# Performance work log

Measured on AMD Instinct MI355X. Metric: run time of the kernel, lower is better.

Reference implementation:

```python
import jax, jax.numpy as jnp
import numpy as np
import math

B, T, C = 2, 2048, 1024
H, DK, DV = 16, 64, 64


def setup_inputs() -> dict:
    key = jax.random.key(0)
    ks = jax.random.split(key, 5)
    # randw(*d) = randn(*d) / sqrt(d[-1])
    x = jax.random.normal(ks[0], (B, T, C), dtype=jnp.float32)
    w_q = jax.random.normal(ks[1], (H, DK, C), dtype=jnp.float32) / math.sqrt(C)
    w_k = jax.random.normal(ks[2], (H, DK, C), dtype=jnp.float32) / math.sqrt(C)
    w_v = jax.random.normal(ks[3], (H, DV, C), dtype=jnp.float32) / math.sqrt(C)
    w_o = jax.random.normal(ks[4], (H * DV, C), dtype=jnp.float32) / math.sqrt(C)
    return {"x": x, "w_q": w_q, "w_k": w_k, "w_v": w_v, "w_o": w_o}


def reference(x, w_q, w_k, w_v, w_o):
    # Full prefill: bs_q.first = 0, bs_q.nb = T, causal=True, dropout=0 (eval).
    dk = w_q.shape[1]
    q = jnp.einsum('ntc,hdc->nhtd', x, w_q)  # [B,H,T,DK]
    k = jnp.einsum('ntc,hdc->nhtd', x, w_k)  # [B,H,T,DK]
    v = jnp.einsum('ntc,hdc->nhtd', x, w_v)  # [B,H,T,DV]
    a = jnp.einsum('nhtd,nhsd->nhts', q, k) / jnp.sqrt(jnp.asarray(dk, x.dtype))
    # amm_generator: mask where query_idx < key_idx (strict upper triangle)
    t = a.shape[-1]
    mask = jnp.arange(t)[:, None] < jnp.arange(t)[None, :]  # [T,T] bool
    a = jnp.where(mask[None, None], jnp.asarray(-jnp.inf, a.dtype), a)
    a = jax.nn.softmax(a, axis=-1)
    y = jnp.einsum('nhts,nhsd->nthd', a, v)  # [B,T,H,DV]
    y = y.reshape(y.shape[0], y.shape[1], -1)  # [B,T,H*DV]
    return y @ w_o  # [B,T,C]
```

## Files before the change

kernel.cpp:

```cpp
#include <hip/hip_runtime.h>
#include <hip/hip_bf16.h>

#define B_ 2
#define T_ 2048
#define C_ 1024
#define H_ 16
#define D_ 64

typedef __attribute__((ext_vector_type(8))) short bf16x8;
typedef __attribute__((ext_vector_type(4))) float f32x4;
typedef __attribute__((ext_vector_type(8))) unsigned short u16x8;
typedef __attribute__((ext_vector_type(2))) unsigned int u32x2;
typedef __attribute__((ext_vector_type(4))) unsigned int u32x4;

__device__ __forceinline__ unsigned short bf1(float a) {
    __bf16 x = (__bf16)a;
    return __builtin_bit_cast(unsigned short, x);
}
__device__ __forceinline__ unsigned int pk2(float a, float b) {
    return (unsigned int)bf1(a) | ((unsigned int)bf1(b) << 16);
}
__device__ __forceinline__ float bf2f(unsigned short u) {
    union { unsigned int u; float f; } v; v.u = (unsigned int)u << 16;
    return v.f;
}

__device__ __forceinline__ void gll16(const void* g, void* l) {
    __builtin_amdgcn_global_load_lds(
        (const __attribute__((address_space(1))) unsigned int*)g,
        (__attribute__((address_space(3))) unsigned int*)l, 16, 0, 0);
}

__global__ __launch_bounds__(256) void prep_x(
    const float* __restrict__ x, unsigned short* __restrict__ xb)
{
    const size_t i = ((size_t)blockIdx.x * 256 + threadIdx.x) * 16;
    float4 f0 = *reinterpret_cast<const float4*>(x + i);
    float4 f1 = *reinterpret_cast<const float4*>(x + i + 4);
    float4 f2 = *reinterpret_cast<const float4*>(x + i + 8);
    float4 f3 = *reinterpret_cast<const float4*>(x + i + 12);
    u32x4 a = {pk2(f0.x, f0.y), pk2(f0.z, f0.w), pk2(f1.x, f1.y), pk2(f1.z, f1.w)};
    u32x4 b = {pk2(f2.x, f2.y), pk2(f2.z, f2.w), pk2(f3.x, f3.y), pk2(f3.z, f3.w)};
    *reinterpret_cast<u32x4*>(xb + i) = a;
    *reinterpret_cast<u32x4*>(xb + i + 8) = b;
}

__global__ __launch_bounds__(256) void prep_w(
    const float* __restrict__ wq, const float* __restrict__ wk,
    const float* __restrict__ wv, unsigned short* __restrict__ wb)
{
    const int bid = blockIdx.x, tid = threadIdx.x;
    const int rb = bid * 4;
    const float* src = (rb < 1024) ? wq + (size_t)rb * 1024
                     : (rb < 2048) ? wk + (size_t)(rb - 1024) * 1024
                                   : wv + (size_t)(rb - 2048) * 1024;
    const float sc = (rb < 1024) ? 0.125f * 1.4426950408889634f : 1.0f;
    const float4* s4 = (const float4*)src;
    u32x2* d = (u32x2*)(wb + (size_t)rb * 1024);
#pragma unroll
    for (int k = 0; k < 4; k++) {
        float4 v = s4[k * 256 + tid];
        u32x2 w;
        w[0] = pk2(v.x * sc, v.y * sc);
        w[1] = pk2(v.z * sc, v.w * sc);
        d[k * 256 + tid] = w;
    }
}

__global__ __launch_bounds__(256) void prep_wo(
    const float* __restrict__ wo, unsigned short* __restrict__ wt)
{
    __shared__ unsigned short tile[64][72];
    const int tk = (blockIdx.x & 15) << 6, tn = (blockIdx.x >> 4) << 6;
    const int r = threadIdx.x >> 2, cb = (threadIdx.x & 3) << 4;
#pragma unroll
    for (int j = 0; j < 4; j++) {
        float4 v = *reinterpret_cast<const float4*>(
            wo + (size_t)(tk + r) * 1024 + tn + cb + j * 4);
        u32x2 w;
        w[0] = pk2(v.x, v.y);
        w[1] = pk2(v.z, v.w);
        *reinterpret_cast<u32x2*>(&tile[r][cb + j * 4]) = w;
    }
    __syncthreads();
    unsigned short buf[16];
#pragma unroll
    for (int j = 0; j < 16; j++) buf[j] = tile[cb + j][r];
    unsigned short* dst = wt + (size_t)(tn + r) * 1024 + tk + cb;
    *reinterpret_cast<u16x8*>(dst) = *reinterpret_cast<u16x8*>(buf);
    *reinterpret_cast<u16x8*>(dst + 8) = *reinterpret_cast<u16x8*>(buf + 8);
}

__global__ __launch_bounds__(256) void qkv_gemm(
    const unsigned short* __restrict__ xb, const unsigned short* __restrict__ wb,
    unsigned short* __restrict__ qkv)
{
    __shared__ __align__(16) unsigned short As[2][128 * 64];
    __shared__ __align__(16) unsigned short Bs[2][128 * 64];
    const int tid = threadIdx.x;
    const int lane = tid & 63, wave = tid >> 6;
    const int g = lane >> 4, c16 = lane & 15;
    const int xcd = blockIdx.x & 7, idx = blockIdx.x >> 3;
    const int bm = (xcd << 2) + idx / 24, bn = idx % 24;
    const int jbase = bn << 7;
    const int which = jbase >> 10;

    const int srow = wave * 32 + (lane >> 3);
    const int swc = ((lane & 7) ^ (lane >> 3)) << 3;
    const unsigned short* asrc = xb + ((size_t)(bm << 7) + srow) * C_ + swc;
    const unsigned short* bsrc = wb + ((size_t)(bn << 7) + srow) * C_ + swc;

    f32x4 acc[4][4];
#pragma unroll
    for (int i = 0; i < 4; i++)
#pragma unroll
        for (int j = 0; j < 4; j++) acc[i][j] = (f32x4){0.f, 0.f, 0.f, 0.f};

    const int wm = (wave >> 1) << 6, wn = (wave & 1) << 6;

    auto stage = [&](int buf, int k0) {
#pragma unroll
        for (int i = 0; i < 4; i++) {
            gll16(asrc + k0 + i * 8 * C_, &As[buf][(wave * 32 + i * 8) << 6]);
            gll16(bsrc + k0 + i * 8 * C_, &Bs[buf][(wave * 32 + i * 8) << 6]);
        }
    };

    stage(0, 0);
    int cur = 0;
    for (int t = 0; t < 16; ++t) {
        __syncthreads();
        if (t < 15) stage(cur ^ 1, (t + 1) << 6);
#pragma unroll
        for (int kk = 0; kk < 2; kk++) {
            bf16x8 af[4], bfv[4];
#pragma unroll
            for (int m = 0; m < 4; m++)
                af[m] = *reinterpret_cast<const bf16x8*>(
                    &As[cur][((wm + m * 16 + c16) << 6) + ((((kk << 2) + g) ^ (c16 & 7)) << 3)]);
#pragma unroll
            for (int n = 0; n < 4; n++)
                bfv[n] = *reinterpret_cast<const bf16x8*>(
                    &Bs[cur][((wn + n * 16 + c16) << 6) + ((((kk << 2) + g) ^ (c16 & 7)) << 3)]);
#pragma unroll
            for (int m = 0; m < 4; m++)
#pragma unroll
                for (int n = 0; n < 4; n++)
                    acc[m][n] = __builtin_amdgcn_mfma_f32_16x16x32_bf16(af[m], bfv[n], acc[m][n], 0, 0, 0);
        }
        cur ^= 1;
    }

    if (which < 2) {
#pragma unroll
        for (int m = 0; m < 4; m++) {
            const int grow = (bm << 7) + wm + m * 16 + (g << 2);
#pragma unroll
            for (int n = 0; n < 4; n++) {
                const int jj = (jbase + wn + n * 16 + c16) & 1023;
                const int h = jj >> 6, d = jj & 63;
#pragma unroll
                for (int r = 0; r < 4; r++) {
                    const int row = grow + r;
                    const int b = row >> 11, t = row & 2047;
                    const size_t off = ((size_t)((which * B_ + b) * H_ + h) * T_ + t) * 64 + d;
                    qkv[off] = bf1(acc[m][n][r]);
                }
            }
        }
    } else {
#pragma unroll
        for (int m = 0; m < 4; m++) {
            const int grow = (bm << 7) + wm + m * 16 + (g << 2);
            const int b = grow >> 11, t = grow & 2047;
#pragma unroll
            for (int n = 0; n < 4; n++) {
                const int jj = (jbase + wn + n * 16 + c16) & 1023;
                const int h = jj >> 6, d = jj & 63;
                u32x2 w;
                w[0] = pk2(acc[m][n][0], acc[m][n][1]);
                w[1] = pk2(acc[m][n][2], acc[m][n][3]);
                const size_t off = ((size_t)((2 * B_ + b) * H_ + h) * 64 + d) * T_ + t;
                *reinterpret_cast<u32x2*>(&qkv[off]) = w;
            }
        }
    }
}

__global__ __launch_bounds__(256) void attn(
    const unsigned short* __restrict__ qkv,
    unsigned short* __restrict__ opA, unsigned short* __restrict__ opB,
    float* __restrict__ lbuf)
{
    __shared__ __align__(16) unsigned short Ks[2][64 * 64];
    __shared__ __align__(16) unsigned short Vt[2][64 * 64];
    __shared__ __align__(16) unsigned short Ps[4][16 * 64];
    const int tid = threadIdx.x, lane = tid & 63, wave = tid >> 6;
    const int g = lane >> 4, c16 = lane & 15;
    const int qt = 31 - (blockIdx.x >> 6);
    const int rem = blockIdx.x & 63;
    const int half = rem >> 5, bh = rem & 31;
    const int b = bh >> 4, h = bh & 15;
    const size_t headoff = (size_t)(b * H_ + h) * T_ * 64;
    const size_t QSZ = (size_t)B_ * H_ * T_ * 64;
    const unsigned short* qp = qkv + headoff;
    const unsigned short* kp = qkv + QSZ + headoff;
    const unsigned short* vTp = qkv + 2 * QSZ + headoff;

    const int nt = qt + 1;
    const int h1 = (nt + 1) >> 1;
    const int itlo = half ? h1 : 0, ithi = half ? nt : h1;

    const int qbase = (qt << 6) + wave * 16;
    bf16x8 qf0, qf1;
    {
        const size_t r0 = (size_t)(qbase + c16) * 64;
        qf0 = *reinterpret_cast<const bf16x8*>(qp + r0 + g * 8);
        qf1 = *reinterpret_cast<const bf16x8*>(qp + r0 + 32 + g * 8);
    }

    float l_lane = 0.f;
    f32x4 acc[4];
#pragma unroll
    for (int i = 0; i < 4; i++) acc[i] = (f32x4){0.f, 0.f, 0.f, 0.f};

    const int srow8 = lane >> 3;
    const int swc = ((lane & 7) ^ srow8) << 3;
    const unsigned short* ksrc = kp + (size_t)(wave * 16 + srow8) * 64 + swc;
    const unsigned short* vsrc = vTp + (size_t)(wave * 16 + srow8) * T_ + swc;

    auto stage = [&](int buf, int s0) {
#pragma unroll
        for (int i = 0; i < 2; i++) {
            gll16(ksrc + (size_t)(s0 + i * 8) * 64, &Ks[buf][(wave * 16 + i * 8) << 6]);
            gll16(vsrc + s0 + (size_t)i * 8 * T_, &Vt[buf][(wave * 16 + i * 8) << 6]);
        }
    };

    if (itlo < ithi) {
        stage(0, itlo << 6);
        int cur = 0;
        for (int it = itlo; it < ithi; ++it) {
            __syncthreads();
            if (it + 1 < ithi) stage(cur ^ 1, (it + 1) << 6);
            const int s0 = it << 6;

            f32x4 sfT[4];
#pragma unroll
            for (int f = 0; f < 4; f++) sfT[f] = (f32x4){0.f, 0.f, 0.f, 0.f};
            __builtin_amdgcn_s_setprio(1);
#pragma unroll
            for (int f = 0; f < 4; f++) {
                const int row = f * 16 + c16;
                const int sw = row & 7;
                bf16x8 k0 = *reinterpret_cast<const bf16x8*>(&Ks[cur][(row << 6) + ((g ^ sw) << 3)]);
                bf16x8 k1 = *reinterpret_cast<const bf16x8*>(&Ks[cur][(row << 6) + (((g + 4) ^ sw) << 3)]);
                sfT[f] = __builtin_amdgcn_mfma_f32_16x16x32_bf16(k0, qf0, sfT[f], 0, 0, 0);
                sfT[f] = __builtin_amdgcn_mfma_f32_16x16x32_bf16(k1, qf1, sfT[f], 0, 0, 0);
            }
            __builtin_amdgcn_s_setprio(0);

            if (it == qt) {
                const int qglob = qbase + c16;
#pragma unroll
                for (int f = 0; f < 4; f++)
#pragma unroll
                    for (int r = 0; r < 4; r++) {
                        const int kv = s0 + f * 16 + g * 4 + r;
                        if (kv > qglob) sfT[f][r] = -1e30f;
                    }
            }

#pragma unroll
            for (int f = 0; f < 4; f++)
#pragma unroll
                for (int r = 0; r < 4; r++) {
                    const float pv = __builtin_amdgcn_exp2f(sfT[f][r] - 16.0f);
                    sfT[f][r] = pv;
                    l_lane += pv;
                }

#pragma unroll
            for (int f = 0; f < 4; f++) {
                u32x2 w;
                w[0] = pk2(sfT[f][0], sfT[f][1]);
                w[1] = pk2(sfT[f][2], sfT[f][3]);
                const int addr = (c16 << 6) + ((((f << 1) + (g >> 1)) ^ (c16 & 7)) << 3) + ((g & 1) << 2);
                *reinterpret_cast<u32x2*>(&Ps[wave][addr]) = w;
            }

            __builtin_amdgcn_s_setprio(1);
#pragma unroll
            for (int ks = 0; ks < 2; ks++) {
                bf16x8 pa = *reinterpret_cast<const bf16x8*>(
                    &Ps[wave][(c16 << 6) + ((((ks << 2) + g) ^ (c16 & 7)) << 3)]);
#pragma unroll
                for (int fd = 0; fd < 4; fd++) {
                    const int d = fd * 16 + c16;
                    bf16x8 vf = *reinterpret_cast<const bf16x8*>(
                        &Vt[cur][(d << 6) + ((((ks << 2) + g) ^ (d & 7)) << 3)]);
                    acc[fd] = __builtin_amdgcn_mfma_f32_16x16x32_bf16(vf, pa, acc[fd], 0, 0, 0);
                }
            }
            __builtin_amdgcn_s_setprio(0);
            cur ^= 1;
        }
    }

    unsigned short* op = half ? opB : opA;
#pragma unroll
    for (int fd = 0; fd < 4; fd++) {
        u32x2 w;
        w[0] = pk2(acc[fd][0], acc[fd][1]);
        w[1] = pk2(acc[fd][2], acc[fd][3]);
        const size_t cy = ((size_t)b * T_ + qbase + c16) * 1024 + h * 64 + fd * 16 + g * 4;
        *reinterpret_cast<u32x2*>(&op[cy]) = w;
    }
    l_lane += __shfl_xor(l_lane, 16, 64);
    l_lane += __shfl_xor(l_lane, 32, 64);
    if (lane < 16)
        lbuf[(size_t)half * (B_ * H_ * T_) + ((size_t)(b * H_ + h)) * T_ + qbase + c16] = l_lane;
}

__global__ __launch_bounds__(256) void combine(
    const unsigned short* __restrict__ opA, const unsigned short* __restrict__ opB,
    const float* __restrict__ lbuf, unsigned short* __restrict__ y)
{
    const size_t i = ((size_t)blockIdx.x * 256 + threadIdx.x) * 8;
    const int hh = (int)((i >> 6) & 15);
    const int t = (int)((i >> 10) & 2047);
    const int bb = (int)(i >> 21);
    const size_t li = ((size_t)(bb * H_ + hh)) * T_ + t;
    const float inv = 1.0f / (lbuf[li] + lbuf[(size_t)B_ * H_ * T_ + li]);
    u16x8 a = *reinterpret_cast<const u16x8*>(opA + i);
    u16x8 c = *reinterpret_cast<const u16x8*>(opB + i);
    unsigned short o[8];
#pragma unroll
    for (int j = 0; j < 8; j++) o[j] = bf1((bf2f(a[j]) + bf2f(c[j])) * inv);
    *reinterpret_cast<u16x8*>(y + i) = *reinterpret_cast<u16x8*>(o);
}

__global__ __launch_bounds__(256) void out_proj(
    const unsigned short* __restrict__ y, const unsigned short* __restrict__ wt,
    float* __restrict__ out)
{
    __shared__ __align__(16) unsigned short As[2][128 * 64];
    __shared__ __align__(16) unsigned short Bs[2][128 * 64];
    const int tid = threadIdx.x;
    const int lane = tid & 63, wave = tid >> 6;
    const int g = lane >> 4, c16 = lane & 15;
    const int xcd = blockIdx.x & 7, idx = blockIdx.x >> 3;
    const int bm = (xcd << 2) + (idx >> 3), bn = idx & 7;
    const int wm = (wave >> 1) << 6, wn = (wave & 1) << 6;

    const int srow = wave * 32 + (lane >> 3);
    const int swc = ((lane & 7) ^ (lane >> 3)) << 3;
    const unsigned short* ysrc = y + ((size_t)(bm << 7) + srow) * 1024 + swc;
    const unsigned short* wsrc = wt + ((size_t)(bn << 7) + srow) * 1024 + swc;

    f32x4 acc[4][4];
#pragma unroll
    for (int i = 0; i < 4; i++)
#pragma unroll
        for (int j = 0; j < 4; j++) acc[i][j] = (f32x4){0.f, 0.f, 0.f, 0.f};

    auto stage = [&](int buf, int k0) {
#pragma unroll
        for (int i = 0; i < 4; i++) {
            gll16(ysrc + k0 + i * 8 * 1024, &As[buf][(wave * 32 + i * 8) << 6]);
            gll16(wsrc + k0 + i * 8 * 1024, &Bs[buf][(wave * 32 + i * 8) << 6]);
        }
    };

    stage(0, 0);
    int cur = 0;
    for (int t = 0; t < 16; ++t) {
        __syncthreads();
        if (t < 15) stage(cur ^ 1, (t + 1) << 6);
#pragma unroll
        for (int kk = 0; kk < 2; kk++) {
            bf16x8 af[4], bfr[4];
#pragma unroll
            for (int m = 0; m < 4; m++)
                af[m] = *reinterpret_cast<const bf16x8*>(
                    &As[cur][((wm + m * 16 + c16) << 6) + ((((kk << 2) + g) ^ (c16 & 7)) << 3)]);
#pragma unroll
            for (int n = 0; n < 4; n++)
                bfr[n] = *reinterpret_cast<const bf16x8*>(
                    &Bs[cur][((wn + n * 16 + c16) << 6) + ((((kk << 2) + g) ^ (c16 & 7)) << 3)]);
#pragma unroll
            for (int m = 0; m < 4; m++)
#pragma unroll
                for (int n = 0; n < 4; n++)
                    acc[m][n] = __builtin_amdgcn_mfma_f32_16x16x32_bf16(af[m], bfr[n], acc[m][n], 0, 0, 0);
        }
        cur ^= 1;
    }

#pragma unroll
    for (int m = 0; m < 4; m++) {
        const int grow = (bm << 7) + wm + m * 16 + (g << 2);
#pragma unroll
        for (int n = 0; n < 4; n++) {
            const int gcol = (bn << 7) + wn + n * 16 + c16;
#pragma unroll
            for (int r = 0; r < 4; r++)
                out[(size_t)(grow + r) * 1024 + gcol] = acc[m][n][r];
        }
    }
}

extern "C" void kernel_launch(void* const* d_in, const int* in_sizes, int n_in,
                              void* d_out, int out_size, void* d_ws, size_t ws_size,
                              hipStream_t stream) {
    const float* x  = (const float*)d_in[0];
    const float* wq = (const float*)d_in[1];
    const float* wk = (const float*)d_in[2];
    const float* wv = (const float*)d_in[3];
    const float* wo = (const float*)d_in[4];
    float* out = (float*)d_out;

    unsigned short* wb   = (unsigned short*)d_ws;
    unsigned short* opB  = (unsigned short*)d_ws;
    unsigned short* y    = opB;
    unsigned short* qkv  = (unsigned short*)d_ws + (size_t)4 * 1024 * 1024;
    unsigned short* wt   = qkv;
    unsigned short* xb   = (unsigned short*)d_out;
    unsigned short* opA  = (unsigned short*)d_out;
    float* lbuf = (float*)((char*)d_out + (size_t)8 * 1024 * 1024);

    prep_x<<<dim3(1024), 256, 0, stream>>>(x, xb);
    prep_w<<<dim3(768), 256, 0, stream>>>(wq, wk, wv, wb);
    qkv_gemm<<<dim3(768), 256, 0, stream>>>(xb, wb, qkv);
    attn<<<dim3(2048), 256, 0, stream>>>(qkv, opA, opB, lbuf);
    combine<<<dim3(4096), 256, 0, stream>>>(opA, opB, lbuf, y);
    prep_wo<<<dim3(256), 256, 0, stream>>>(wo, wt);
    out_proj<<<dim3(256), 256, 0, stream>>>(y, wt, out);
}
```

Baseline: 125.1 us.

## Replace double-buffered GEMM staging with single-buffer BK=32, halve out_proj tile

Both GEMMs drop their double-buffered 64-wide K staging with XOR swizzle in favour of a single 32-wide K buffer, loaded synchronously between two barriers each iteration. The smaller LDS footprint is meant to raise occupancy, so other resident blocks hide load latency instead of in-block prefetch. out_proj also moves to 128x64 tiles with 512 blocks to fill more CUs. The costs are no in-block overlap of loads and MFMA, twice as many barriers, and likely LDS bank conflicts now that the swizzle is gone.

```diff
diff --git a/kernel.cpp b/kernel.cpp
--- a/kernel.cpp
+++ b/kernel.cpp
@@ -95,8 +95,8 @@
     const unsigned short* __restrict__ xb, const unsigned short* __restrict__ wb,
     unsigned short* __restrict__ qkv)
 {
-    __shared__ __align__(16) unsigned short As[2][128 * 64];
-    __shared__ __align__(16) unsigned short Bs[2][128 * 64];
+    __shared__ __align__(16) unsigned short As[128 * 32];
+    __shared__ __align__(16) unsigned short Bs[128 * 32];
     const int tid = threadIdx.x;
     const int lane = tid & 63, wave = tid >> 6;
     const int g = lane >> 4, c16 = lane & 15;
@@ -105,10 +105,9 @@
     const int jbase = bn << 7;
     const int which = jbase >> 10;
 
-    const int srow = wave * 32 + (lane >> 3);
-    const int swc = ((lane & 7) ^ (lane >> 3)) << 3;
-    const unsigned short* asrc = xb + ((size_t)(bm << 7) + srow) * C_ + swc;
-    const unsigned short* bsrc = wb + ((size_t)(bn << 7) + srow) * C_ + swc;
+    const int srow = lane >> 2, sch = (lane & 3) << 3;
+    const unsigned short* asrc = xb + ((size_t)(bm << 7) + wave * 32 + srow) * C_ + sch;
+    const unsigned short* bsrc = wb + ((size_t)(bn << 7) + wave * 32 + srow) * C_ + sch;
 
     f32x4 acc[4][4];
 #pragma unroll
@@ -118,37 +117,27 @@
 
     const int wm = (wave >> 1) << 6, wn = (wave & 1) << 6;
 
-    auto stage = [&](int buf, int k0) {
-#pragma unroll
-        for (int i = 0; i < 4; i++) {
-            gll16(asrc + k0 + i * 8 * C_, &As[buf][(wave * 32 + i * 8) << 6]);
-            gll16(bsrc + k0 + i * 8 * C_, &Bs[buf][(wave * 32 + i * 8) << 6]);
-        }
-    };
-
-    stage(0, 0);
-    int cur = 0;
-    for (int t = 0; t < 16; ++t) {
+    for (int t = 0; t < 32; ++t) {
+        const int k0 = t << 5;
         __syncthreads();
-        if (t < 15) stage(cur ^ 1, (t + 1) << 6);
-#pragma unroll
-        for (int kk = 0; kk < 2; kk++) {
-            bf16x8 af[4], bfv[4];
-#pragma unroll
-            for (int m = 0; m < 4; m++)
-                af[m] = *reinterpret_cast<const bf16x8*>(
-                    &As[cur][((wm + m * 16 + c16) << 6) + ((((kk << 2) + g) ^ (c16 & 7)) << 3)]);
+        gll16(asrc + k0,           &As[(wave * 32) << 5]);
+        gll16(asrc + k0 + 16 * C_, &As[(wave * 32 + 16) << 5]);
+        gll16(bsrc + k0,           &Bs[(wave * 32) << 5]);
+        gll16(bsrc + k0 + 16 * C_, &Bs[(wave * 32 + 16) << 5]);
+        __syncthreads();
+
+        bf16x8 af[4], bfv[4];
+#pragma unroll
+        for (int m = 0; m < 4; m++)
+            af[m] = *reinterpret_cast<const bf16x8*>(&As[((wm + m * 16 + c16) << 5) + g * 8]);
+#pragma unroll
+        for (int n = 0; n < 4; n++)
+            bfv[n] = *reinterpret_cast<const bf16x8*>(&Bs[((wn + n * 16 + c16) << 5) + g * 8]);
+#pragma unroll
+        for (int m = 0; m < 4; m++)
 #pragma unroll
             for (int n = 0; n < 4; n++)
-                bfv[n] = *reinterpret_cast<const bf16x8*>(
-                    &Bs[cur][((wn + n * 16 + c16) << 6) + ((((kk << 2) + g) ^ (c16 & 7)) << 3)]);
-#pragma unroll
-            for (int m = 0; m < 4; m++)
-#pragma unroll
-                for (int n = 0; n < 4; n++)
-                    acc[m][n] = __builtin_amdgcn_mfma_f32_16x16x32_bf16(af[m], bfv[n], acc[m][n], 0, 0, 0);
-        }
-        cur ^= 1;
+                acc[m][n] = __builtin_amdgcn_mfma_f32_16x16x32_bf16(af[m], bfv[n], acc[m][n], 0, 0, 0);
     }
 
     if (which < 2) {
@@ -344,65 +333,53 @@
     const unsigned short* __restrict__ y, const unsigned short* __restrict__ wt,
     float* __restrict__ out)
 {
-    __shared__ __align__(16) unsigned short As[2][128 * 64];
-    __shared__ __align__(16) unsigned short Bs[2][128 * 64];
+    __shared__ __align__(16) unsigned short As[128 * 32];
+    __shared__ __align__(16) unsigned short Bs[64 * 32];
     const int tid = threadIdx.x;
     const int lane = tid & 63, wave = tid >> 6;
     const int g = lane >> 4, c16 = lane & 15;
     const int xcd = blockIdx.x & 7, idx = blockIdx.x >> 3;
-    const int bm = (xcd << 2) + (idx >> 3), bn = idx & 7;
-    const int wm = (wave >> 1) << 6, wn = (wave & 1) << 6;
-
-    const int srow = wave * 32 + (lane >> 3);
-    const int swc = ((lane & 7) ^ (lane >> 3)) << 3;
-    const unsigned short* ysrc = y + ((size_t)(bm << 7) + srow) * 1024 + swc;
-    const unsigned short* wsrc = wt + ((size_t)(bn << 7) + srow) * 1024 + swc;
-
-    f32x4 acc[4][4];
+    const int bm = (xcd << 2) + (idx >> 4), bn = idx & 15;
+    const int wm = (wave >> 1) << 6, wn = (wave & 1) << 5;
+
+    const int srow = lane >> 2, sch = (lane & 3) << 3;
+    const unsigned short* ysrc = y + ((size_t)(bm << 7) + wave * 32 + srow) * 1024 + sch;
+    const unsigned short* wsrc = wt + ((size_t)(bn << 6) + wave * 16 + srow) * 1024 + sch;
+
+    f32x4 acc[4][2];
 #pragma unroll
     for (int i = 0; i < 4; i++)
 #pragma unroll
-        for (int j = 0; j < 4; j++) acc[i][j] = (f32x4){0.f, 0.f, 0.f, 0.f};
-
-    auto stage = [&](int buf, int k0) {
-#pragma unroll
-        for (int i = 0; i < 4; i++) {
-            gll16(ysrc + k0 + i * 8 * 1024, &As[buf][(wave * 32 + i * 8) << 6]);
-            gll16(wsrc + k0 + i * 8 * 1024, &Bs[buf][(wave * 32 + i * 8) << 6]);
-        }
-    };
-
-    stage(0, 0);
-    int cur = 0;
-    for (int t = 0; t < 16; ++t) {
+        for (int j = 0; j < 2; j++) acc[i][j] = (f32x4){0.f, 0.f, 0.f, 0.f};
+
+    for (int t = 0; t < 32; ++t) {
+        const int k0 = t << 5;
         __syncthreads();
-        if (t < 15) stage(cur ^ 1, (t + 1) << 6);
-#pragma unroll
-        for (int kk = 0; kk < 2; kk++) {
-            bf16x8 af[4], bfr[4];
-#pragma unroll
-            for (int m = 0; m < 4; m++)
-                af[m] = *reinterpret_cast<const bf16x8*>(
-                    &As[cur][((wm + m * 16 + c16) << 6) + ((((kk << 2) + g) ^ (c16 & 7)) << 3)]);
-#pragma unroll
-            for (int n = 0; n < 4; n++)
-                bfr[n] = *reinterpret_cast<const bf16x8*>(
-                    &Bs[cur][((wn + n * 16 + c16) << 6) + ((((kk << 2) + g) ^ (c16 & 7)) << 3)]);
-#pragma unroll
-            for (int m = 0; m < 4; m++)
-#pragma unroll
-                for (int n = 0; n < 4; n++)
-                    acc[m][n] = __builtin_amdgcn_mfma_f32_16x16x32_bf16(af[m], bfr[n], acc[m][n], 0, 0, 0);
-        }
-        cur ^= 1;
+        gll16(ysrc + k0,            &As[(wave * 32) << 5]);
+        gll16(ysrc + k0 + 16 * 1024, &As[(wave * 32 + 16) << 5]);
+        gll16(wsrc + k0,            &Bs[(wave * 16) << 5]);
+        __syncthreads();
+
+        bf16x8 af[4], bfr[2];
+#pragma unroll
+        for (int m = 0; m < 4; m++)
+            af[m] = *reinterpret_cast<const bf16x8*>(&As[((wm + m * 16 + c16) << 5) + g * 8]);
+#pragma unroll
+        for (int n = 0; n < 2; n++)
+            bfr[n] = *reinterpret_cast<const bf16x8*>(&Bs[((wn + n * 16 + c16) << 5) + g * 8]);
+#pragma unroll
+        for (int m = 0; m < 4; m++)
+#pragma unroll
+            for (int n = 0; n < 2; n++)
+                acc[m][n] = __builtin_amdgcn_mfma_f32_16x16x32_bf16(af[m], bfr[n], acc[m][n], 0, 0, 0);
     }
 
 #pragma unroll
     for (int m = 0; m < 4; m++) {
         const int grow = (bm << 7) + wm + m * 16 + (g << 2);
 #pragma unroll
-        for (int n = 0; n < 4; n++) {
-            const int gcol = (bn << 7) + wn + n * 16 + c16;
+        for (int n = 0; n < 2; n++) {
+            const int gcol = (bn << 6) + wn + n * 16 + c16;
 #pragma unroll
             for (int r = 0; r < 4; r++)
                 out[(size_t)(grow + r) * 1024 + gcol] = acc[m][n][r];
@@ -435,5 +412,5 @@
     attn<<<dim3(2048), 256, 0, stream>>>(qkv, opA, opB, lbuf);
     combine<<<dim3(4096), 256, 0, stream>>>(opA, opB, lbuf, y);
     prep_wo<<<dim3(256), 256, 0, stream>>>(wo, wt);
-    out_proj<<<dim3(256), 256, 0, stream>>>(y, wt, out);
-}
+    out_proj<<<dim3(512), 256, 0, stream>>>(y, wt, out);
+}
```

Result: faster. 117.8 us (-5.9%).
